# Kernel tuning notes

Measured on AMD Instinct MI355X. Metric: run time of the kernel, lower is better.

The kernel has to match this reference:

```python
import jax, jax.numpy as jnp
import numpy as np

B_SZ, N_IN, N_CTX, UNITS, RANK = 4096, 4096, 512, 4096, 256


def setup_inputs() -> dict:
    key = jax.random.key(0)
    ks = jax.random.split(key, 8)
    inputs = jax.random.normal(ks[0], (B_SZ, N_IN), dtype=jnp.float32)
    context = jax.random.normal(ks[1], (B_SZ, N_CTX), dtype=jnp.float32)
    # Orthogonal-ish init approximated by scaled normals (math-equivalent shapes)
    U = jax.random.normal(ks[2], (N_IN, RANK), dtype=jnp.float32) / np.sqrt(N_IN)
    S = jax.random.uniform(ks[3], (RANK,), dtype=jnp.float32, minval=0.5, maxval=1.5)
    V = jax.random.normal(ks[4], (UNITS, RANK), dtype=jnp.float32) / np.sqrt(UNITS)
    W = jax.random.normal(ks[5], (N_CTX, RANK), dtype=jnp.float32) / np.sqrt(N_CTX)
    B = jnp.zeros((RANK,), dtype=jnp.float32)
    bias = jnp.zeros((UNITS,), dtype=jnp.float32)
    return {"inputs": inputs, "context": context, "U": U, "S": S, "V": V, "W": W, "B": B, "bias": bias}


def reference(inputs, context, U, S, V, W, B, bias):
    # chi[b,r] = sigmoid(context @ W + B)
    chi = jax.nn.sigmoid(context @ W + B)                  # [B, R]
    # Original: kernel[b,n,m] = sum_r U[n,r]*S[r]*chi[b,r]*V[m,r];
    # out[b,m] = sum_n x[b,n]*kernel[b,n,m]. Algebraically equal to:
    t = (inputs @ U) * (S * chi)                           # [B, R]
    out = t @ V.T + bias                                   # first '+ self.bias'
    out = out + bias                                       # 'outputs += self.bias' (use_bias=True)
    return jax.nn.relu(out)
```

## Files before the change

kernel.cpp:

```cpp
#include <hip/hip_runtime.h>

#define B_SZ 4096
#define N_IN 4096
#define N_CTX 512
#define UNITS 4096
#define RANK 256
#define ZSPLIT 8

typedef __attribute__((ext_vector_type(8))) __bf16 bf16x8;
typedef __attribute__((ext_vector_type(4))) float f32x4;
typedef __attribute__((ext_vector_type(8))) unsigned short ushort8;

__device__ __forceinline__ unsigned short f2bf(float f) {
    unsigned int u = __float_as_uint(f);
    u += 0x7FFFu + ((u >> 16) & 1u);
    return (unsigned short)(u >> 16);
}
__device__ __forceinline__ unsigned short f2bf_fast(float f) {
    return (unsigned short)((__float_as_uint(f) + 0x8000u) >> 16);
}
__device__ __forceinline__ float bf2f(unsigned short h) {
    return __uint_as_float(((unsigned int)h) << 16);
}
__device__ __forceinline__ void gload_lds16(const unsigned short* g, unsigned short* l) {
    __builtin_amdgcn_global_load_lds(
        (const __attribute__((address_space(1))) unsigned int*)g,
        (__attribute__((address_space(3))) unsigned int*)l, 16, 0, 0);
}
__device__ __forceinline__ bf16x8 ldfrag(const unsigned short* p) {
    ushort8 t = *(const ushort8*)p;
    return __builtin_bit_cast(bf16x8, t);
}
__device__ __forceinline__ ushort8 cvt8u(float4 lo, float4 hi) {
    ushort8 t = { f2bf_fast(lo.x), f2bf_fast(lo.y), f2bf_fast(lo.z), f2bf_fast(lo.w),
                  f2bf_fast(hi.x), f2bf_fast(hi.y), f2bf_fast(hi.z), f2bf_fast(hi.w) };
    return t;
}
#define MFMA(a, b, c) __builtin_amdgcn_mfma_f32_16x16x32_bf16((a), (b), (c), 0, 0, 0)

__global__ void prep(const float* __restrict__ U, const float* __restrict__ W,
                     const float* __restrict__ V,
                     unsigned short* __restrict__ UT, unsigned short* __restrict__ WT,
                     unsigned short* __restrict__ Vb) {
    __shared__ unsigned short t[64][66];
    int bid = blockIdx.x, tid = threadIdx.x;
    if (bid < 288) {
        const float* src; unsigned short* dst; int R, C, rb, cb;
        if (bid < 256) { src = U; dst = UT; R = N_IN; C = RANK; rb = (bid & 63) * 64; cb = (bid >> 6) * 64; }
        else { int b = bid - 256; src = W; dst = WT; R = N_CTX; C = RANK; rb = (b & 7) * 64; cb = (b >> 3) * 64; }
        int r = tid >> 4, c4 = (tid & 15) * 4;
        for (int i = 0; i < 4; i++) {
            float4 v = *(const float4*)(src + (size_t)(rb + r + i * 16) * C + cb + c4);
            t[r + i * 16][c4 + 0] = f2bf(v.x);
            t[r + i * 16][c4 + 1] = f2bf(v.y);
            t[r + i * 16][c4 + 2] = f2bf(v.z);
            t[r + i * 16][c4 + 3] = f2bf(v.w);
        }
        __syncthreads();
        int c = tid >> 3, r8 = (tid & 7) * 8;
        for (int j = 0; j < 2; j++) {
            int cc = c + j * 32;
            ushort8 o;
            for (int k = 0; k < 8; k++) o[k] = t[r8 + k][cc];
            *(ushort8*)(dst + (size_t)(cb + cc) * R + rb + r8) = o;
        }
    } else {
        size_t base = (size_t)(bid - 288) * 2048 + (size_t)tid * 8;
        float4 a = *(const float4*)(V + base);
        float4 b = *(const float4*)(V + base + 4);
        ushort8 o = { f2bf(a.x), f2bf(a.y), f2bf(a.z), f2bf(a.w),
                      f2bf(b.x), f2bf(b.y), f2bf(b.z), f2bf(b.w) };
        *(ushort8*)(Vb + base) = o;
    }
}

__launch_bounds__(256, 4)
__global__ void k1_chi(const float* __restrict__ ctx, const unsigned short* __restrict__ WT,
                       const float* __restrict__ S, const float* __restrict__ Bb,
                       unsigned short* __restrict__ Schi) {
    __shared__ unsigned short Bs[64 * 512];
    int tid = threadIdx.x, wv = tid >> 6, lane = tid & 63;
    int ln15 = lane & 15, quad = lane >> 4;
    int n0 = blockIdx.x * 64, mbase = blockIdx.y * 64;
    #pragma unroll
    for (int i = 0; i < 16; i++) {
        int linear = i * 256 + tid;
        int r = linear >> 6, c = linear & 63;
        ushort8 v = *(const ushort8*)(WT + (size_t)(n0 + r) * N_CTX + c * 8);
        *(ushort8*)(Bs + r * 512 + ((c ^ (r & 7)) * 8)) = v;
    }
    __syncthreads();
    int m0 = mbase + wv * 16;
    const float* Xp = ctx + (size_t)(m0 + ln15) * N_CTX + quad * 8;
    f32x4 acc[4] = {};
    float4 a[2][2];
    a[0][0] = *(const float4*)(Xp); a[0][1] = *(const float4*)(Xp + 4);
    #pragma unroll
    for (int kt = 0; kt < 16; kt++) {
        int cur = kt & 1, nxt = cur ^ 1;
        if (kt < 15) {
            int ko = (kt + 1) * 32;
            a[nxt][0] = *(const float4*)(Xp + ko); a[nxt][1] = *(const float4*)(Xp + ko + 4);
        }
        bf16x8 bfr[4];
        int sw8 = ((4 * kt + quad) ^ (ln15 & 7)) * 8;
        #pragma unroll
        for (int j = 0; j < 4; j++) bfr[j] = ldfrag(Bs + (j * 16 + ln15) * 512 + sw8);
        bf16x8 af = __builtin_bit_cast(bf16x8, cvt8u(a[cur][0], a[cur][1]));
        #pragma unroll
        for (int j = 0; j < 4; j++) acc[j] = MFMA(af, bfr[j], acc[j]);
    }
    #pragma unroll
    for (int j = 0; j < 4; j++) {
        int col = n0 + j * 16 + ln15;
        float sv = S[col], bv = Bb[col];
        #pragma unroll
        for (int r = 0; r < 4; r++) {
            int row = m0 + quad * 4 + r;
            float x = acc[j][r] + bv;
            Schi[(size_t)row * RANK + col] = f2bf_fast(sv / (1.f + __expf(-x)));
        }
    }
}

__launch_bounds__(256, 2)
__global__ void k2_t0(const float* __restrict__ X, const unsigned short* __restrict__ UT,
                      unsigned short* __restrict__ T0p) {
    __shared__ __align__(16) unsigned short Bs[2][256 * 64];
    int tid = threadIdx.x, wv = tid >> 6, lane = tid & 63;
    int ln15 = lane & 15, quad = lane >> 4;
    int mbase = blockIdx.x * 64;
    int z = blockIdx.y;
    int kbase = z * 512;
    const float* Xp = X + (size_t)(mbase + wv * 16 + ln15) * N_IN + kbase + quad * 8;

    #pragma unroll
    for (int i = 0; i < 8; i++) {
        int linear = i * 256 + tid;
        int r = linear >> 3, cs = linear & 7;
        int gc = cs ^ (r & 7);
        gload_lds16(UT + (size_t)r * N_IN + kbase + gc * 8, &Bs[0][linear * 8]);
    }
    float4 a[2][2][2];
    #pragma unroll
    for (int kh = 0; kh < 2; kh++) {
        a[0][kh][0] = *(const float4*)(Xp + kh * 32);
        a[0][kh][1] = *(const float4*)(Xp + kh * 32 + 4);
    }
    f32x4 acc[16] = {};
    #pragma unroll
    for (int kt = 0; kt < 8; kt++) {
        int cur = kt & 1, nxt = cur ^ 1;
        __syncthreads();
        if (kt < 7) {
            int k0 = (kt + 1) * 64;
            #pragma unroll
            for (int i = 0; i < 8; i++) {
                int linear = i * 256 + tid;
                int r = linear >> 3, cs = linear & 7;
                int gc = cs ^ (r & 7);
                gload_lds16(UT + (size_t)r * N_IN + kbase + k0 + gc * 8, &Bs[nxt][linear * 8]);
            }
            #pragma unroll
            for (int kh = 0; kh < 2; kh++) {
                a[nxt][kh][0] = *(const float4*)(Xp + k0 + kh * 32);
                a[nxt][kh][1] = *(const float4*)(Xp + k0 + kh * 32 + 4);
            }
        }
        #pragma unroll
        for (int kh = 0; kh < 2; kh++) {
            bf16x8 af = __builtin_bit_cast(bf16x8, cvt8u(a[cur][kh][0], a[cur][kh][1]));
            int g = kh * 4 + quad;
            int sw8 = (g ^ (ln15 & 7)) * 8;
            #pragma unroll
            for (int j = 0; j < 16; j++) {
                bf16x8 bfr = ldfrag(&Bs[cur][(j * 16 + ln15) * 64 + sw8]);
                acc[j] = MFMA(af, bfr, acc[j]);
            }
        }
    }
    unsigned short* P = T0p + (size_t)z * B_SZ * RANK + (size_t)(mbase + wv * 16) * RANK;
    #pragma unroll
    for (int j = 0; j < 16; j++) {
        int col = j * 16 + ln15;
        #pragma unroll
        for (int r = 0; r < 4; r++) {
            int row = quad * 4 + r;
            P[(size_t)row * RANK + col] = f2bf_fast(acc[j][r]);
        }
    }
}

__global__ void e_red(const unsigned short* __restrict__ T0p, const unsigned short* __restrict__ Schi,
                      unsigned short* __restrict__ T) {
    int i = blockIdx.x * 256 + threadIdx.x;
    const size_t stride = (size_t)B_SZ * RANK;
    float a[8] = {};
    for (int z = 0; z < ZSPLIT; z++) {
        ushort8 p = *(const ushort8*)(T0p + z * stride + (size_t)i * 8);
        for (int k = 0; k < 8; k++) a[k] += bf2f(p[k]);
    }
    ushort8 s = *(const ushort8*)(Schi + (size_t)i * 8);
    ushort8 o;
    for (int k = 0; k < 8; k++) o[k] = f2bf_fast(a[k] * bf2f(s[k]));
    *(ushort8*)(T + (size_t)i * 8) = o;
}

__launch_bounds__(256, 4)
__global__ void k3_out(const unsigned short* __restrict__ T, const unsigned short* __restrict__ Vb,
                       const float* __restrict__ bias, float* __restrict__ out) {
    __shared__ unsigned short Bs[64 * 256];
    int tid = threadIdx.x, wv = tid >> 6, lane = tid & 63;
    int ln15 = lane & 15, quad = lane >> 4;
    int n0 = blockIdx.x * 64, mbase = blockIdx.y * 128;
    #pragma unroll
    for (int i = 0; i < 8; i++) {
        int linear = i * 256 + tid;
        int r = linear >> 5, c = linear & 31;
        ushort8 v = *(const ushort8*)(Vb + (size_t)(n0 + r) * RANK + c * 8);
        *(ushort8*)(Bs + r * 256 + ((c ^ (r & 7)) * 8)) = v;
    }
    __syncthreads();
    int m0 = mbase + wv * 32;
    const unsigned short* Ap  = T + (size_t)(m0 + ln15) * RANK + quad * 8;
    const unsigned short* Ap2 = Ap + (size_t)16 * RANK;
    f32x4 acc[2][4] = {};
    ushort8 a[2][2];
    a[0][0] = *(const ushort8*)(Ap);
    a[0][1] = *(const ushort8*)(Ap2);
    #pragma unroll
    for (int kt = 0; kt < 8; kt++) {
        int cur = kt & 1, nxt = cur ^ 1;
        if (kt < 7) {
            int ko = (kt + 1) * 32;
            a[nxt][0] = *(const ushort8*)(Ap + ko);
            a[nxt][1] = *(const ushort8*)(Ap2 + ko);
        }
        bf16x8 bfr[4];
        int sw8 = ((4 * kt + quad) ^ (ln15 & 7)) * 8;
        #pragma unroll
        for (int j = 0; j < 4; j++) bfr[j] = ldfrag(Bs + (j * 16 + ln15) * 256 + sw8);
        bf16x8 af0 = __builtin_bit_cast(bf16x8, a[cur][0]);
        bf16x8 af1 = __builtin_bit_cast(bf16x8, a[cur][1]);
        #pragma unroll
        for (int j = 0; j < 4; j++) {
            acc[0][j] = MFMA(af0, bfr[j], acc[0][j]);
            acc[1][j] = MFMA(af1, bfr[j], acc[1][j]);
        }
    }
    #pragma unroll
    for (int j = 0; j < 4; j++) {
        int col = n0 + j * 16 + ln15;
        float bv = 2.f * bias[col];
        #pragma unroll
        for (int i = 0; i < 2; i++)
            #pragma unroll
            for (int r = 0; r < 4; r++) {
                int row = m0 + i * 16 + quad * 4 + r;
                float v = acc[i][j][r] + bv;
                out[(size_t)row * UNITS + col] = fmaxf(v, 0.f);
            }
    }
}

extern "C" void kernel_launch(void* const* d_in, const int* in_sizes, int n_in,
                              void* d_out, int out_size, void* d_ws, size_t ws_size,
                              hipStream_t stream) {
    (void)in_sizes; (void)n_in; (void)out_size; (void)ws_size;
    const float* inputs  = (const float*)d_in[0];
    const float* context = (const float*)d_in[1];
    const float* U       = (const float*)d_in[2];
    const float* S       = (const float*)d_in[3];
    const float* V       = (const float*)d_in[4];
    const float* W       = (const float*)d_in[5];
    const float* Bb      = (const float*)d_in[6];
    const float* bias    = (const float*)d_in[7];
    float* out = (float*)d_out;

    char* ws = (char*)d_ws;
    size_t o = 0;
    unsigned short* UT   = (unsigned short*)(ws + o); o += (size_t)RANK * N_IN * 2;
    unsigned short* WT   = (unsigned short*)(ws + o); o += (size_t)RANK * N_CTX * 2;
    unsigned short* Vb   = (unsigned short*)(ws + o); o += (size_t)UNITS * RANK * 2;
    unsigned short* Schi = (unsigned short*)(ws + o); o += (size_t)B_SZ * RANK * 2;
    unsigned short* T    = (unsigned short*)(ws + o); o += (size_t)B_SZ * RANK * 2;
    unsigned short* T0p  = (unsigned short*)(ws + o); o += (size_t)ZSPLIT * B_SZ * RANK * 2;

    prep<<<800, 256, 0, stream>>>(U, W, V, UT, WT, Vb);
    k2_t0<<<dim3(64, 8), 256, 0, stream>>>(inputs, UT, T0p);
    k1_chi<<<dim3(4, 64), 256, 0, stream>>>(context, WT, S, Bb, Schi);
    e_red<<<(B_SZ * RANK) / (256 * 8), 256, 0, stream>>>(T0p, Schi, T);
    k3_out<<<dim3(64, 32), 256, 0, stream>>>(T, Vb, bias, out);
}
```

Measured before the change: 181.0 us.

## Merge chi and partial-T GEMMs into one launch with 2x2 warp tiling

Folds the context@W sigmoid kernel and the split-K inputs@U kernel into one launch, with blocks 0-511 doing the split-K GEMM and blocks 512-767 computing Schi. The GEMM warps now use a 2x2 layout (32 rows by 128 columns each), so each LDS B fragment feeds two MFMAs instead of one. The aim is to remove one launch and the gap between kernels, let the small chi work fill idle CUs, and halve LDS fragment reads per MFMA. In exchange, the chi blocks inherit the larger shared-memory allocation and the 2-waves-per-SIMD launch bound, and the GEMM warps hold more A-operand registers.

```diff
diff --git a/kernel.cpp b/kernel.cpp
--- a/kernel.cpp
+++ b/kernel.cpp
@@ -74,119 +74,128 @@
     }
 }
 
-__launch_bounds__(256, 4)
-__global__ void k1_chi(const float* __restrict__ ctx, const unsigned short* __restrict__ WT,
-                       const float* __restrict__ S, const float* __restrict__ Bb,
-                       unsigned short* __restrict__ Schi) {
-    __shared__ unsigned short Bs[64 * 512];
+__launch_bounds__(256, 2)
+__global__ void k12(const float* __restrict__ X, const unsigned short* __restrict__ UT,
+                    unsigned short* __restrict__ T0p,
+                    const float* __restrict__ ctx, const unsigned short* __restrict__ WT,
+                    const float* __restrict__ S, const float* __restrict__ Bb,
+                    unsigned short* __restrict__ Schi) {
+    __shared__ __align__(16) unsigned short smem[2 * 256 * 64];
     int tid = threadIdx.x, wv = tid >> 6, lane = tid & 63;
     int ln15 = lane & 15, quad = lane >> 4;
-    int n0 = blockIdx.x * 64, mbase = blockIdx.y * 64;
-    #pragma unroll
-    for (int i = 0; i < 16; i++) {
-        int linear = i * 256 + tid;
-        int r = linear >> 6, c = linear & 63;
-        ushort8 v = *(const ushort8*)(WT + (size_t)(n0 + r) * N_CTX + c * 8);
-        *(ushort8*)(Bs + r * 512 + ((c ^ (r & 7)) * 8)) = v;
-    }
-    __syncthreads();
-    int m0 = mbase + wv * 16;
-    const float* Xp = ctx + (size_t)(m0 + ln15) * N_CTX + quad * 8;
-    f32x4 acc[4] = {};
-    float4 a[2][2];
-    a[0][0] = *(const float4*)(Xp); a[0][1] = *(const float4*)(Xp + 4);
-    #pragma unroll
-    for (int kt = 0; kt < 16; kt++) {
-        int cur = kt & 1, nxt = cur ^ 1;
-        if (kt < 15) {
-            int ko = (kt + 1) * 32;
-            a[nxt][0] = *(const float4*)(Xp + ko); a[nxt][1] = *(const float4*)(Xp + ko + 4);
-        }
-        bf16x8 bfr[4];
-        int sw8 = ((4 * kt + quad) ^ (ln15 & 7)) * 8;
-        #pragma unroll
-        for (int j = 0; j < 4; j++) bfr[j] = ldfrag(Bs + (j * 16 + ln15) * 512 + sw8);
-        bf16x8 af = __builtin_bit_cast(bf16x8, cvt8u(a[cur][0], a[cur][1]));
-        #pragma unroll
-        for (int j = 0; j < 4; j++) acc[j] = MFMA(af, bfr[j], acc[j]);
-    }
-    #pragma unroll
-    for (int j = 0; j < 4; j++) {
-        int col = n0 + j * 16 + ln15;
-        float sv = S[col], bv = Bb[col];
-        #pragma unroll
-        for (int r = 0; r < 4; r++) {
-            int row = m0 + quad * 4 + r;
-            float x = acc[j][r] + bv;
-            Schi[(size_t)row * RANK + col] = f2bf_fast(sv / (1.f + __expf(-x)));
-        }
-    }
-}
-
-__launch_bounds__(256, 2)
-__global__ void k2_t0(const float* __restrict__ X, const unsigned short* __restrict__ UT,
-                      unsigned short* __restrict__ T0p) {
-    __shared__ __align__(16) unsigned short Bs[2][256 * 64];
-    int tid = threadIdx.x, wv = tid >> 6, lane = tid & 63;
-    int ln15 = lane & 15, quad = lane >> 4;
-    int mbase = blockIdx.x * 64;
-    int z = blockIdx.y;
-    int kbase = z * 512;
-    const float* Xp = X + (size_t)(mbase + wv * 16 + ln15) * N_IN + kbase + quad * 8;
-
-    #pragma unroll
-    for (int i = 0; i < 8; i++) {
-        int linear = i * 256 + tid;
-        int r = linear >> 3, cs = linear & 7;
-        int gc = cs ^ (r & 7);
-        gload_lds16(UT + (size_t)r * N_IN + kbase + gc * 8, &Bs[0][linear * 8]);
-    }
-    float4 a[2][2][2];
-    #pragma unroll
-    for (int kh = 0; kh < 2; kh++) {
-        a[0][kh][0] = *(const float4*)(Xp + kh * 32);
-        a[0][kh][1] = *(const float4*)(Xp + kh * 32 + 4);
-    }
-    f32x4 acc[16] = {};
-    #pragma unroll
-    for (int kt = 0; kt < 8; kt++) {
-        int cur = kt & 1, nxt = cur ^ 1;
+
+    if (blockIdx.x < 512) {
+        int mbase = (blockIdx.x & 63) * 64;
+        int z = blockIdx.x >> 6;
+        int kbase = z * 512;
+        int wm = wv & 1, wn = wv >> 1;
+        const float* Xp  = X + (size_t)(mbase + wm * 32 + ln15) * N_IN + kbase + quad * 8;
+        const float* Xp2 = Xp + (size_t)16 * N_IN;
+
+        #pragma unroll
+        for (int i = 0; i < 8; i++) {
+            int linear = i * 256 + tid;
+            int r = linear >> 3, cs = linear & 7;
+            int gc = cs ^ (r & 7);
+            gload_lds16(UT + (size_t)r * N_IN + kbase + gc * 8, &smem[linear * 8]);
+        }
+        float4 a[2][2][2][2];
+        #pragma unroll
+        for (int kh = 0; kh < 2; kh++) {
+            a[0][0][kh][0] = *(const float4*)(Xp + kh * 32);
+            a[0][0][kh][1] = *(const float4*)(Xp + kh * 32 + 4);
+            a[0][1][kh][0] = *(const float4*)(Xp2 + kh * 32);
+            a[0][1][kh][1] = *(const float4*)(Xp2 + kh * 32 + 4);
+        }
+        f32x4 acc[2][8] = {};
+        #pragma unroll
+        for (int kt = 0; kt < 8; kt++) {
+            int cur = kt & 1, nxt = cur ^ 1;
+            __syncthreads();
+            if (kt < 7) {
+                int k0 = (kt + 1) * 64;
+                #pragma unroll
+                for (int i = 0; i < 8; i++) {
+                    int linear = i * 256 + tid;
+                    int r = linear >> 3, cs = linear & 7;
+                    int gc = cs ^ (r & 7);
+                    gload_lds16(UT + (size_t)r * N_IN + kbase + k0 + gc * 8,
+                                &smem[nxt * 16384 + linear * 8]);
+                }
+                #pragma unroll
+                for (int kh = 0; kh < 2; kh++) {
+                    a[nxt][0][kh][0] = *(const float4*)(Xp + k0 + kh * 32);
+                    a[nxt][0][kh][1] = *(const float4*)(Xp + k0 + kh * 32 + 4);
+                    a[nxt][1][kh][0] = *(const float4*)(Xp2 + k0 + kh * 32);
+                    a[nxt][1][kh][1] = *(const float4*)(Xp2 + k0 + kh * 32 + 4);
+                }
+            }
+            #pragma unroll
+            for (int kh = 0; kh < 2; kh++) {
+                int sw8 = ((kh * 4 + quad) ^ (ln15 & 7)) * 8;
+                bf16x8 af0 = __builtin_bit_cast(bf16x8, cvt8u(a[cur][0][kh][0], a[cur][0][kh][1]));
+                bf16x8 af1 = __builtin_bit_cast(bf16x8, cvt8u(a[cur][1][kh][0], a[cur][1][kh][1]));
+                #pragma unroll
+                for (int j = 0; j < 8; j++) {
+                    bf16x8 bfr = ldfrag(&smem[cur * 16384 + (wn * 128 + j * 16 + ln15) * 64 + sw8]);
+                    acc[0][j] = MFMA(af0, bfr, acc[0][j]);
+                    acc[1][j] = MFMA(af1, bfr, acc[1][j]);
+                }
+            }
+        }
+        unsigned short* P = T0p + (size_t)z * B_SZ * RANK;
+        #pragma unroll
+        for (int rg = 0; rg < 2; rg++)
+            #pragma unroll
+            for (int j = 0; j < 8; j++) {
+                int col = wn * 128 + j * 16 + ln15;
+                #pragma unroll
+                for (int r = 0; r < 4; r++) {
+                    int row = mbase + wm * 32 + rg * 16 + quad * 4 + r;
+                    P[(size_t)row * RANK + col] = f2bf_fast(acc[rg][j][r]);
+                }
+            }
+    } else {
+        int bid = blockIdx.x - 512;
+        int n0 = (bid & 3) * 64, mbase = (bid >> 2) * 64;
+        #pragma unroll
+        for (int i = 0; i < 16; i++) {
+            int linear = i * 256 + tid;
+            int r = linear >> 6, c = linear & 63;
+            ushort8 v = *(const ushort8*)(WT + (size_t)(n0 + r) * N_CTX + c * 8);
+            *(ushort8*)(&smem[r * 512 + ((c ^ (r & 7)) * 8)]) = v;
+        }
         __syncthreads();
-        if (kt < 7) {
-            int k0 = (kt + 1) * 64;
-            #pragma unroll
-            for (int i = 0; i < 8; i++) {
-                int linear = i * 256 + tid;
-                int r = linear >> 3, cs = linear & 7;
-                int gc = cs ^ (r & 7);
-                gload_lds16(UT + (size_t)r * N_IN + kbase + k0 + gc * 8, &Bs[nxt][linear * 8]);
-            }
-            #pragma unroll
-            for (int kh = 0; kh < 2; kh++) {
-                a[nxt][kh][0] = *(const float4*)(Xp + k0 + kh * 32);
-                a[nxt][kh][1] = *(const float4*)(Xp + k0 + kh * 32 + 4);
-            }
-        }
-        #pragma unroll
-        for (int kh = 0; kh < 2; kh++) {
-            bf16x8 af = __builtin_bit_cast(bf16x8, cvt8u(a[cur][kh][0], a[cur][kh][1]));
-            int g = kh * 4 + quad;
-            int sw8 = (g ^ (ln15 & 7)) * 8;
-            #pragma unroll
-            for (int j = 0; j < 16; j++) {
-                bf16x8 bfr = ldfrag(&Bs[cur][(j * 16 + ln15) * 64 + sw8]);
-                acc[j] = MFMA(af, bfr, acc[j]);
-            }
-        }
-    }
-    unsigned short* P = T0p + (size_t)z * B_SZ * RANK + (size_t)(mbase + wv * 16) * RANK;
-    #pragma unroll
-    for (int j = 0; j < 16; j++) {
-        int col = j * 16 + ln15;
-        #pragma unroll
-        for (int r = 0; r < 4; r++) {
-            int row = quad * 4 + r;
-            P[(size_t)row * RANK + col] = f2bf_fast(acc[j][r]);
+        int m0 = mbase + wv * 16;
+        const float* Xp = ctx + (size_t)(m0 + ln15) * N_CTX + quad * 8;
+        f32x4 acc[4] = {};
+        float4 a[2][2];
+        a[0][0] = *(const float4*)(Xp); a[0][1] = *(const float4*)(Xp + 4);
+        #pragma unroll
+        for (int kt = 0; kt < 16; kt++) {
+            int cur = kt & 1, nxt = cur ^ 1;
+            if (kt < 15) {
+                int ko = (kt + 1) * 32;
+                a[nxt][0] = *(const float4*)(Xp + ko); a[nxt][1] = *(const float4*)(Xp + ko + 4);
+            }
+            bf16x8 bfr[4];
+            int sw8 = ((4 * kt + quad) ^ (ln15 & 7)) * 8;
+            #pragma unroll
+            for (int j = 0; j < 4; j++) bfr[j] = ldfrag(&smem[(j * 16 + ln15) * 512 + sw8]);
+            bf16x8 af = __builtin_bit_cast(bf16x8, cvt8u(a[cur][0], a[cur][1]));
+            #pragma unroll
+            for (int j = 0; j < 4; j++) acc[j] = MFMA(af, bfr[j], acc[j]);
+        }
+        #pragma unroll
+        for (int j = 0; j < 4; j++) {
+            int col = n0 + j * 16 + ln15;
+            float sv = S[col], bv = Bb[col];
+            #pragma unroll
+            for (int r = 0; r < 4; r++) {
+                int row = m0 + quad * 4 + r;
+                float x = acc[j][r] + bv;
+                Schi[(size_t)row * RANK + col] = f2bf_fast(sv / (1.f + __expf(-x)));
+            }
         }
     }
 }
@@ -287,8 +296,7 @@
     unsigned short* T0p  = (unsigned short*)(ws + o); o += (size_t)ZSPLIT * B_SZ * RANK * 2;
 
     prep<<<800, 256, 0, stream>>>(U, W, V, UT, WT, Vb);
-    k2_t0<<<dim3(64, 8), 256, 0, stream>>>(inputs, UT, T0p);
-    k1_chi<<<dim3(4, 64), 256, 0, stream>>>(context, WT, S, Bb, Schi);
+    k12<<<768, 256, 0, stream>>>(inputs, UT, T0p, context, WT, S, Bb, Schi);
     e_red<<<(B_SZ * RANK) / (256 * 8), 256, 0, stream>>>(T0p, Schi, T);
     k3_out<<<dim3(64, 32), 256, 0, stream>>>(T, Vb, bias, out);
 }
```

New measurement: 185.7 us. 2.6% more time.
